# Performance work log

Measured on AMD Instinct MI355X. Metric: run time of the kernel, lower is better.

## Reference

```python
import jax, jax.numpy as jnp
import numpy as np

B, C_IN, C_OUT, DK, N = 4, 64, 64, 64, 4096

def setup_inputs() -> dict:
    key = jax.random.key(0)
    kx, kq, kk, kv = jax.random.split(key, 4)
    return {
        "x": jax.random.normal(kx, (B, C_IN, N), dtype=jnp.float32),
        "Wq": jax.random.normal(kq, (DK, C_IN), dtype=jnp.float32) * 0.1,
        "Wk": jax.random.normal(kk, (DK, C_IN), dtype=jnp.float32) * 0.1,
        "Wv": jax.random.normal(kv, (C_OUT, C_IN), dtype=jnp.float32) * 0.1,
    }

def reference(x, Wq, Wk, Wv):
    # Conv1d(kernel=1, bias=False) == channel matmul.
    q = jnp.einsum('dc,bcn->bnd', Wq, x)          # (B, N, dk)  (transpose(1,2))
    k = jnp.einsum('dc,bcn->bdn', Wk, x)          # (B, dk, N)
    v = jnp.einsum('oc,bcn->bon', Wv, x)          # (B, C_out, N)
    dk = q.shape[2]
    scores = jnp.einsum('bnd,bdm->bnm', q, k) / jnp.sqrt(jnp.asarray(dk, x.dtype))  # (B, N, N)
    attn = jax.nn.softmax(scores, axis=1)         # NOTE: softmax over dim=1 (columns), as in the torch code
    return jnp.einsum('bon,bnm->bom', v, attn)    # (B, C_out, N)
```

## Files before the change

### kernel.cpp

```cpp
#include <hip/hip_runtime.h>
#include <hip/hip_bf16.h>
#include <math.h>

#define N_ 4096
#define B_ 4
#define C_ 64
#define MT 64
#define NT 128
#define STEPS (N_ / NT)
#define QSCALE 0.1803368801111137f

typedef __attribute__((ext_vector_type(8))) short bf16x8;
typedef __attribute__((ext_vector_type(4))) float f32x4;
#define MFMA(a, b, c) __builtin_amdgcn_mfma_f32_16x16x32_bf16(a, b, c, 0, 0, 0)

#if __has_builtin(__builtin_amdgcn_exp2f)
#define EXP2(x) __builtin_amdgcn_exp2f(x)
#else
#define EXP2(x) __expf((x) * 0.6931471805599453f)
#endif

static __device__ __forceinline__ uint hi_bits(float f) {
    return (__float_as_uint(f) + 0x8000u) >> 16;
}
static __device__ __forceinline__ float hi_val(float f) {
    return __uint_as_float((__float_as_uint(f) + 0x8000u) & 0xFFFF0000u);
}

__global__ __launch_bounds__(256) void qkv_mfma(
    const float* __restrict__ x,  const float* __restrict__ Wq,
    const float* __restrict__ Wk, const float* __restrict__ Wv,
    ushort* __restrict__ Qh, ushort* __restrict__ Kh, ushort* __restrict__ Vh)
{
    __shared__ float xs[C_][33];

    const int b   = blockIdx.x / (N_ / 32);
    const int n0  = (blockIdx.x % (N_ / 32)) * 32;
    const int tid = threadIdx.x;
    const int w   = tid >> 6;
    const int l   = tid & 63;
    const int lr  = l & 15;
    const int lg  = l >> 4;

    #pragma unroll
    for (int it = 0; it < 2; ++it) {
        const int i = tid + it * 256;
        const int row = i >> 3, q = i & 7;
        const float4 a = *(const float4*)(x + ((size_t)b * C_ + row) * N_ + n0 + q * 4);
        xs[row][q * 4 + 0] = a.x; xs[row][q * 4 + 1] = a.y;
        xs[row][q * 4 + 2] = a.z; xs[row][q * 4 + 3] = a.w;
    }

    bf16x8 wh[3][2], wl[3][2];
    #pragma unroll
    for (int i = 0; i < 3; ++i) {
        const int rt  = w * 3 + i;
        const int mat = rt >> 2;
        const int dt  = rt & 3;
        const float* __restrict__ W = (mat == 0) ? Wq : ((mat == 1) ? Wk : Wv);
        const float scale = (mat == 0) ? QSCALE : 1.0f;
        #pragma unroll
        for (int ks = 0; ks < 2; ++ks) {
            const float4* p = (const float4*)(W + (dt * 16 + lr) * C_ + ks * 32 + lg * 8);
            float4 f0 = p[0], f1 = p[1];
            float v[8] = {f0.x, f0.y, f0.z, f0.w, f1.x, f1.y, f1.z, f1.w};
            bf16x8 ht, lt;
            #pragma unroll
            for (int j = 0; j < 8; ++j) {
                const float f = v[j] * scale;
                const float h = hi_val(f);
                ht[j] = (short)(__float_as_uint(h) >> 16);
                lt[j] = (short)hi_bits(f - h);
            }
            wh[i][ks] = ht; wl[i][ks] = lt;
        }
    }
    __syncthreads();

    #pragma unroll
    for (int nt = 0; nt < 2; ++nt) {
        bf16x8 xh[2], xl[2];
        #pragma unroll
        for (int ks = 0; ks < 2; ++ks) {
            bf16x8 ht, lt;
            #pragma unroll
            for (int j = 0; j < 8; ++j) {
                const float f = xs[ks * 32 + lg * 8 + j][nt * 16 + lr];
                const float h = hi_val(f);
                ht[j] = (short)(__float_as_uint(h) >> 16);
                lt[j] = (short)hi_bits(f - h);
            }
            xh[ks] = ht; xl[ks] = lt;
        }

        #pragma unroll
        for (int i = 0; i < 3; ++i) {
            const int rt  = w * 3 + i;
            const int mat = rt >> 2;
            const int dt  = rt & 3;
            f32x4 acc = (f32x4){0.f, 0.f, 0.f, 0.f};
            if (mat < 2) {
                #pragma unroll
                for (int ks = 0; ks < 2; ++ks) {
                    acc = MFMA(wh[i][ks], xh[ks], acc);
                    acc = MFMA(wh[i][ks], xl[ks], acc);
                    acc = MFMA(wl[i][ks], xh[ks], acc);
                }
                ushort* __restrict__ H = mat ? Kh : Qh;
                const size_t base = ((size_t)b * N_ + n0 + nt * 16 + lr) * C_ + dt * 16 + lg * 4;
                *(uint2*)(H + base) = make_uint2((hi_bits(acc[1]) << 16) | hi_bits(acc[0]),
                                                 (hi_bits(acc[3]) << 16) | hi_bits(acc[2]));
            } else {
                #pragma unroll
                for (int ks = 0; ks < 2; ++ks) {
                    acc = MFMA(xh[ks], wh[i][ks], acc);
                    acc = MFMA(xl[ks], wh[i][ks], acc);
                    acc = MFMA(xh[ks], wl[i][ks], acc);
                }
                const size_t base = ((size_t)b * C_ + dt * 16 + lr) * N_ + n0 + nt * 16 + lg * 4;
                *(uint2*)(Vh + base) = make_uint2((hi_bits(acc[1]) << 16) | hi_bits(acc[0]),
                                                  (hi_bits(acc[3]) << 16) | hi_bits(acc[2]));
            }
        }
    }
}

__global__ __launch_bounds__(256) void attn_mfma(
    const ushort* __restrict__ Qh, const ushort* __restrict__ Kh,
    const ushort* __restrict__ Vh, float* __restrict__ out)
{
    __shared__ ushort Em[2][MT * NT];
    __shared__ float red[4][MT];

    const int bid = blockIdx.x;
    const int b   = (bid & 7) >> 1;
    const int mt  = (bid & 1) + ((bid >> 3) << 1);
    const int tid = threadIdx.x;
    const int w   = tid >> 6;
    const int l   = tid & 63;
    const int lr  = l & 15;
    const int lg  = l >> 4;

    const int m0 = mt * MT;

    bf16x8 khf[4][2];
    #pragma unroll
    for (int f = 0; f < 4; ++f)
        #pragma unroll
        for (int ks = 0; ks < 2; ++ks)
            khf[f][ks] = *(const bf16x8*)(Kh + ((size_t)b * N_ + m0 + f * 16 + lr) * C_ + ks * 32 + lg * 8);

    f32x4 oacc[4];
    #pragma unroll
    for (int f = 0; f < 4; ++f) oacc[f] = (f32x4){0.f, 0.f, 0.f, 0.f};
    float den[4] = {0.f, 0.f, 0.f, 0.f};

    bf16x8 qcur[2][2];
    #pragma unroll
    for (int nt2 = 0; nt2 < 2; ++nt2)
        #pragma unroll
        for (int ks = 0; ks < 2; ++ks)
            qcur[nt2][ks] = *(const bf16x8*)(Qh + ((size_t)b * N_ + w * 32 + nt2 * 16 + lr) * C_ + ks * 32 + lg * 8);

    for (int t = 0; t < STEPS; ++t) {
        const int nbase = t * NT;
        const int buf   = t & 1;

        bf16x8 vh[4];
        #pragma unroll
        for (int ks = 0; ks < 4; ++ks)
            vh[ks] = *(const bf16x8*)(Vh + ((size_t)b * C_ + w * 16 + lr) * N_ + nbase + ks * 32 + lg * 8);

        f32x4 s2[2][4];
        #pragma unroll
        for (int nt2 = 0; nt2 < 2; ++nt2)
            #pragma unroll
            for (int f = 0; f < 4; ++f) s2[nt2][f] = (f32x4){0.f, 0.f, 0.f, 0.f};
        #pragma unroll
        for (int ks = 0; ks < 2; ++ks)
            #pragma unroll
            for (int nt2 = 0; nt2 < 2; ++nt2)
                #pragma unroll
                for (int f = 0; f < 4; ++f)
                    s2[nt2][f] = MFMA(qcur[nt2][ks], khf[f][ks], s2[nt2][f]);

        const int tn = (t + 1 < STEPS) ? (t + 1) : t;
        bf16x8 qnext[2][2];
        #pragma unroll
        for (int nt2 = 0; nt2 < 2; ++nt2)
            #pragma unroll
            for (int ks = 0; ks < 2; ++ks)
                qnext[nt2][ks] = *(const bf16x8*)(Qh + ((size_t)b * N_ + tn * NT + w * 32 + nt2 * 16 + lr) * C_ + ks * 32 + lg * 8);

        #pragma unroll
        for (int nt2 = 0; nt2 < 2; ++nt2)
            #pragma unroll
            for (int f = 0; f < 4; ++f) {
                const float e0 = EXP2(s2[nt2][f][0]);
                const float e1 = EXP2(s2[nt2][f][1]);
                const float e2 = EXP2(s2[nt2][f][2]);
                const float e3 = EXP2(s2[nt2][f][3]);
                den[f] += (e0 + e1) + (e2 + e3);
                const uint u0 = __float_as_uint(e0) + 0x8000u;
                const uint u1 = __float_as_uint(e1) + 0x8000u;
                const uint u2 = __float_as_uint(e2) + 0x8000u;
                const uint u3 = __float_as_uint(e3) + 0x8000u;
                const uint2 pk = make_uint2((u1 & 0xFFFF0000u) | (u0 >> 16),
                                            (u3 & 0xFFFF0000u) | (u2 >> 16));
                const int row = f * 16 + lr;
                const int g   = w * 4 + nt2 * 2 + (lg >> 1);
                *(uint2*)&Em[buf][row * NT + (((g + row) & 15) << 3) + ((lg & 1) << 2)] = pk;
            }
        __syncthreads();

        #pragma unroll
        for (int ks = 0; ks < 4; ++ks)
            #pragma unroll
            for (int f = 0; f < 4; ++f) {
                const int row = f * 16 + lr;
                const bf16x8 eb = *(const bf16x8*)&Em[buf][row * NT + (((ks * 4 + lg + row) & 15) << 3)];
                oacc[f] = MFMA(vh[ks], eb, oacc[f]);
            }

        #pragma unroll
        for (int nt2 = 0; nt2 < 2; ++nt2) {
            qcur[nt2][0] = qnext[nt2][0];
            qcur[nt2][1] = qnext[nt2][1];
        }
    }

    #pragma unroll
    for (int f = 0; f < 4; ++f) {
        den[f] += __shfl_xor(den[f], 16);
        den[f] += __shfl_xor(den[f], 32);
    }
    __syncthreads();
    if (lg == 0)
        #pragma unroll
        for (int f = 0; f < 4; ++f) red[w][f * 16 + lr] = den[f];
    __syncthreads();

    float inv[4];
    #pragma unroll
    for (int f = 0; f < 4; ++f) {
        const int m = f * 16 + lr;
        inv[f] = __builtin_amdgcn_rcpf(red[0][m] + red[1][m] + red[2][m] + red[3][m]);
    }

    #pragma unroll
    for (int f = 0; f < 4; ++f)
        #pragma unroll
        for (int r = 0; r < 4; ++r) {
            const int o = w * 16 + lg * 4 + r;
            out[((size_t)b * C_ + o) * N_ + m0 + f * 16 + lr] = oacc[f][r] * inv[f];
        }
}

extern "C" void kernel_launch(void* const* d_in, const int* in_sizes, int n_in,
                              void* d_out, int out_size, void* d_ws, size_t ws_size,
                              hipStream_t stream)
{
    const float* x  = (const float*)d_in[0];
    const float* Wq = (const float*)d_in[1];
    const float* Wk = (const float*)d_in[2];
    const float* Wv = (const float*)d_in[3];
    float* out = (float*)d_out;

    const size_t NE = (size_t)B_ * N_ * C_;
    ushort* Qh = (ushort*)d_ws;
    ushort* Kh = Qh + NE;
    ushort* Vh = Kh + NE;

    qkv_mfma<<<B_ * (N_ / 32), 256, 0, stream>>>(x, Wq, Wk, Wv, Qh, Kh, Vh);
    attn_mfma<<<B_ * (N_ / MT), 256, 0, stream>>>(Qh, Kh, Vh, out);
}
```

Baseline: 107.4 us.

## Warp-specialize attention kernel into score producer and PV consumer waves

Expands the attention block to 16 waves: 8 waves compute QK^T scores, exp and denominators for the next tile into a double-buffered LDS buffer, while 8 waves consume the current tile for the V·P MFMAs, splitting the n range in halves. Partial outputs from the two halves are reduced through LDS at the end. This aims to overlap exp/score work with the PV matmul and raise per-CU wave occupancy, at the cost of a larger block, extra LDS reduction and tighter register limits.

```diff
diff --git a/kernel.cpp b/kernel.cpp
--- a/kernel.cpp
+++ b/kernel.cpp
@@ -125,12 +125,12 @@
     }
 }
 
-__global__ __launch_bounds__(256) void attn_mfma(
+__global__ __launch_bounds__(1024) void attn_mfma(
     const ushort* __restrict__ Qh, const ushort* __restrict__ Kh,
     const ushort* __restrict__ Vh, float* __restrict__ out)
 {
     __shared__ ushort Em[2][MT * NT];
-    __shared__ float red[4][MT];
+    __shared__ float red[8][MT];
 
     const int bid = blockIdx.x;
     const int b   = (bid & 7) >> 1;
@@ -140,120 +140,152 @@
     const int l   = tid & 63;
     const int lr  = l & 15;
     const int lg  = l >> 4;
-
-    const int m0 = mt * MT;
+    const int m0  = mt * MT;
+
+    const bool sW = (w < 8);
+    const int pw  = w & 7;
+    const int ot  = pw & 3;
+    const int nh  = pw >> 2;
 
     bf16x8 khf[4][2];
-    #pragma unroll
-    for (int f = 0; f < 4; ++f)
-        #pragma unroll
-        for (int ks = 0; ks < 2; ++ks)
-            khf[f][ks] = *(const bf16x8*)(Kh + ((size_t)b * N_ + m0 + f * 16 + lr) * C_ + ks * 32 + lg * 8);
-
-    f32x4 oacc[4];
+    float  den[4] = {0.f, 0.f, 0.f, 0.f};
+    f32x4  oacc[4];
     #pragma unroll
     for (int f = 0; f < 4; ++f) oacc[f] = (f32x4){0.f, 0.f, 0.f, 0.f};
-    float den[4] = {0.f, 0.f, 0.f, 0.f};
-
-    bf16x8 qcur[2][2];
-    #pragma unroll
-    for (int nt2 = 0; nt2 < 2; ++nt2)
+    bf16x8 vcur[2];
+
+    if (sW) {
+        #pragma unroll
+        for (int f = 0; f < 4; ++f)
+            #pragma unroll
+            for (int ks = 0; ks < 2; ++ks)
+                khf[f][ks] = *(const bf16x8*)(Kh + ((size_t)b * N_ + m0 + f * 16 + lr) * C_ + ks * 32 + lg * 8);
+
+        bf16x8 q[2];
         #pragma unroll
         for (int ks = 0; ks < 2; ++ks)
-            qcur[nt2][ks] = *(const bf16x8*)(Qh + ((size_t)b * N_ + w * 32 + nt2 * 16 + lr) * C_ + ks * 32 + lg * 8);
+            q[ks] = *(const bf16x8*)(Qh + ((size_t)b * N_ + w * 16 + lr) * C_ + ks * 32 + lg * 8);
+        f32x4 s[4];
+        #pragma unroll
+        for (int f = 0; f < 4; ++f) s[f] = (f32x4){0.f, 0.f, 0.f, 0.f};
+        __builtin_amdgcn_s_setprio(1);
+        #pragma unroll
+        for (int ks = 0; ks < 2; ++ks)
+            #pragma unroll
+            for (int f = 0; f < 4; ++f) s[f] = MFMA(q[ks], khf[f][ks], s[f]);
+        __builtin_amdgcn_s_setprio(0);
+        #pragma unroll
+        for (int f = 0; f < 4; ++f) {
+            const float e0 = EXP2(s[f][0]), e1 = EXP2(s[f][1]);
+            const float e2 = EXP2(s[f][2]), e3 = EXP2(s[f][3]);
+            den[f] += (e0 + e1) + (e2 + e3);
+            const uint u0 = __float_as_uint(e0) + 0x8000u;
+            const uint u1 = __float_as_uint(e1) + 0x8000u;
+            const uint u2 = __float_as_uint(e2) + 0x8000u;
+            const uint u3 = __float_as_uint(e3) + 0x8000u;
+            const int row = f * 16 + lr;
+            const int g   = w * 2 + (lg >> 1);
+            *(uint2*)&Em[0][row * NT + (((g + row) & 15) << 3) + ((lg & 1) << 2)] =
+                make_uint2((u1 & 0xFFFF0000u) | (u0 >> 16), (u3 & 0xFFFF0000u) | (u2 >> 16));
+        }
+    } else {
+        #pragma unroll
+        for (int k2 = 0; k2 < 2; ++k2)
+            vcur[k2] = *(const bf16x8*)(Vh + ((size_t)b * C_ + ot * 16 + lr) * N_ + nh * 64 + k2 * 32 + lg * 8);
+    }
+    __syncthreads();
 
     for (int t = 0; t < STEPS; ++t) {
-        const int nbase = t * NT;
-        const int buf   = t & 1;
-
-        bf16x8 vh[4];
-        #pragma unroll
-        for (int ks = 0; ks < 4; ++ks)
-            vh[ks] = *(const bf16x8*)(Vh + ((size_t)b * C_ + w * 16 + lr) * N_ + nbase + ks * 32 + lg * 8);
-
-        f32x4 s2[2][4];
-        #pragma unroll
-        for (int nt2 = 0; nt2 < 2; ++nt2)
-            #pragma unroll
-            for (int f = 0; f < 4; ++f) s2[nt2][f] = (f32x4){0.f, 0.f, 0.f, 0.f};
-        #pragma unroll
-        for (int ks = 0; ks < 2; ++ks)
-            #pragma unroll
-            for (int nt2 = 0; nt2 < 2; ++nt2)
-                #pragma unroll
-                for (int f = 0; f < 4; ++f)
-                    s2[nt2][f] = MFMA(qcur[nt2][ks], khf[f][ks], s2[nt2][f]);
-
-        const int tn = (t + 1 < STEPS) ? (t + 1) : t;
-        bf16x8 qnext[2][2];
-        #pragma unroll
-        for (int nt2 = 0; nt2 < 2; ++nt2)
-            #pragma unroll
-            for (int ks = 0; ks < 2; ++ks)
-                qnext[nt2][ks] = *(const bf16x8*)(Qh + ((size_t)b * N_ + tn * NT + w * 32 + nt2 * 16 + lr) * C_ + ks * 32 + lg * 8);
-
-        #pragma unroll
-        for (int nt2 = 0; nt2 < 2; ++nt2)
-            #pragma unroll
-            for (int f = 0; f < 4; ++f) {
-                const float e0 = EXP2(s2[nt2][f][0]);
-                const float e1 = EXP2(s2[nt2][f][1]);
-                const float e2 = EXP2(s2[nt2][f][2]);
-                const float e3 = EXP2(s2[nt2][f][3]);
-                den[f] += (e0 + e1) + (e2 + e3);
-                const uint u0 = __float_as_uint(e0) + 0x8000u;
-                const uint u1 = __float_as_uint(e1) + 0x8000u;
-                const uint u2 = __float_as_uint(e2) + 0x8000u;
-                const uint u3 = __float_as_uint(e3) + 0x8000u;
-                const uint2 pk = make_uint2((u1 & 0xFFFF0000u) | (u0 >> 16),
-                                            (u3 & 0xFFFF0000u) | (u2 >> 16));
-                const int row = f * 16 + lr;
-                const int g   = w * 4 + nt2 * 2 + (lg >> 1);
-                *(uint2*)&Em[buf][row * NT + (((g + row) & 15) << 3) + ((lg & 1) << 2)] = pk;
-            }
+        if (sW) {
+            if (t + 1 < STEPS) {
+                bf16x8 q[2];
+                #pragma unroll
+                for (int ks = 0; ks < 2; ++ks)
+                    q[ks] = *(const bf16x8*)(Qh + ((size_t)b * N_ + (t + 1) * NT + w * 16 + lr) * C_ + ks * 32 + lg * 8);
+                f32x4 s[4];
+                #pragma unroll
+                for (int f = 0; f < 4; ++f) s[f] = (f32x4){0.f, 0.f, 0.f, 0.f};
+                __builtin_amdgcn_s_setprio(1);
+                #pragma unroll
+                for (int ks = 0; ks < 2; ++ks)
+                    #pragma unroll
+                    for (int f = 0; f < 4; ++f) s[f] = MFMA(q[ks], khf[f][ks], s[f]);
+                __builtin_amdgcn_s_setprio(0);
+                const int buf = (t + 1) & 1;
+                #pragma unroll
+                for (int f = 0; f < 4; ++f) {
+                    const float e0 = EXP2(s[f][0]), e1 = EXP2(s[f][1]);
+                    const float e2 = EXP2(s[f][2]), e3 = EXP2(s[f][3]);
+                    den[f] += (e0 + e1) + (e2 + e3);
+                    const uint u0 = __float_as_uint(e0) + 0x8000u;
+                    const uint u1 = __float_as_uint(e1) + 0x8000u;
+                    const uint u2 = __float_as_uint(e2) + 0x8000u;
+                    const uint u3 = __float_as_uint(e3) + 0x8000u;
+                    const int row = f * 16 + lr;
+                    const int g   = w * 2 + (lg >> 1);
+                    *(uint2*)&Em[buf][row * NT + (((g + row) & 15) << 3) + ((lg & 1) << 2)] =
+                        make_uint2((u1 & 0xFFFF0000u) | (u0 >> 16), (u3 & 0xFFFF0000u) | (u2 >> 16));
+                }
+            }
+        } else {
+            const int tv = (t + 1 < STEPS) ? t + 1 : t;
+            bf16x8 vnext[2];
+            #pragma unroll
+            for (int k2 = 0; k2 < 2; ++k2)
+                vnext[k2] = *(const bf16x8*)(Vh + ((size_t)b * C_ + ot * 16 + lr) * N_ + (size_t)tv * NT + nh * 64 + k2 * 32 + lg * 8);
+            __builtin_amdgcn_s_setprio(1);
+            #pragma unroll
+            for (int k2 = 0; k2 < 2; ++k2)
+                #pragma unroll
+                for (int f = 0; f < 4; ++f) {
+                    const int row = f * 16 + lr;
+                    const int lgc = (nh * 2 + k2) * 4 + lg;
+                    const bf16x8 eb = *(const bf16x8*)&Em[t & 1][row * NT + (((lgc + row) & 15) << 3)];
+                    oacc[f] = MFMA(vcur[k2], eb, oacc[f]);
+                }
+            __builtin_amdgcn_s_setprio(0);
+            vcur[0] = vnext[0]; vcur[1] = vnext[1];
+        }
         __syncthreads();
-
-        #pragma unroll
-        for (int ks = 0; ks < 4; ++ks)
-            #pragma unroll
-            for (int f = 0; f < 4; ++f) {
-                const int row = f * 16 + lr;
-                const bf16x8 eb = *(const bf16x8*)&Em[buf][row * NT + (((ks * 4 + lg + row) & 15) << 3)];
-                oacc[f] = MFMA(vh[ks], eb, oacc[f]);
-            }
-
-        #pragma unroll
-        for (int nt2 = 0; nt2 < 2; ++nt2) {
-            qcur[nt2][0] = qnext[nt2][0];
-            qcur[nt2][1] = qnext[nt2][1];
-        }
-    }
-
-    #pragma unroll
-    for (int f = 0; f < 4; ++f) {
-        den[f] += __shfl_xor(den[f], 16);
-        den[f] += __shfl_xor(den[f], 32);
+    }
+
+    if (sW) {
+        #pragma unroll
+        for (int f = 0; f < 4; ++f) {
+            den[f] += __shfl_xor(den[f], 16);
+            den[f] += __shfl_xor(den[f], 32);
+        }
+        if (lg == 0)
+            #pragma unroll
+            for (int f = 0; f < 4; ++f) red[w][f * 16 + lr] = den[f];
+    } else if (nh == 1) {
+        float* scr = (float*)&Em[0][0];
+        #pragma unroll
+        for (int f = 0; f < 4; ++f)
+            #pragma unroll
+            for (int r = 0; r < 4; ++r)
+                scr[(ot * 16 + lg * 4 + r) * 65 + f * 16 + lr] = oacc[f][r];
     }
     __syncthreads();
-    if (lg == 0)
-        #pragma unroll
-        for (int f = 0; f < 4; ++f) red[w][f * 16 + lr] = den[f];
-    __syncthreads();
-
-    float inv[4];
-    #pragma unroll
-    for (int f = 0; f < 4; ++f) {
-        const int m = f * 16 + lr;
-        inv[f] = __builtin_amdgcn_rcpf(red[0][m] + red[1][m] + red[2][m] + red[3][m]);
-    }
-
-    #pragma unroll
-    for (int f = 0; f < 4; ++f)
-        #pragma unroll
-        for (int r = 0; r < 4; ++r) {
-            const int o = w * 16 + lg * 4 + r;
-            out[((size_t)b * C_ + o) * N_ + m0 + f * 16 + lr] = oacc[f][r] * inv[f];
-        }
+
+    if (!sW && nh == 0) {
+        const float* scr = (const float*)&Em[0][0];
+        float inv[4];
+        #pragma unroll
+        for (int f = 0; f < 4; ++f) {
+            const int m = f * 16 + lr;
+            inv[f] = __builtin_amdgcn_rcpf(red[0][m] + red[1][m] + red[2][m] + red[3][m] +
+                                           red[4][m] + red[5][m] + red[6][m] + red[7][m]);
+        }
+        #pragma unroll
+        for (int f = 0; f < 4; ++f)
+            #pragma unroll
+            for (int r = 0; r < 4; ++r) {
+                const int o = ot * 16 + lg * 4 + r;
+                out[((size_t)b * C_ + o) * N_ + m0 + f * 16 + lr] =
+                    (oacc[f][r] + scr[o * 65 + f * 16 + lr]) * inv[f];
+            }
+    }
 }
 
 extern "C" void kernel_launch(void* const* d_in, const int* in_sizes, int n_in,
@@ -272,5 +304,5 @@
     ushort* Vh = Kh + NE;
 
     qkv_mfma<<<B_ * (N_ / 32), 256, 0, stream>>>(x, Wq, Wk, Wv, Qh, Kh, Vh);
-    attn_mfma<<<B_ * (N_ / MT), 256, 0, stream>>>(Qh, Kh, Vh, out);
-}
+    attn_mfma<<<B_ * (N_ / MT), 1024, 0, stream>>>(Qh, Kh, Vh, out);
+}
```

Result: slower. 110.0 us (+2.4%).

## Split attention key dimension across eight waves with 32x32 MFMA and register transpose

Applied to the files above, without the earlier changes.

The attention kernel now gives each block 32 output columns and splits the 4096-long reduction over 8 waves. Each wave computes scores with 32x32x16 bf16 MFMAs and transposes the exponentials into B-operand layout using cross-lane shuffles, so the LDS staging and per-step barrier are gone. A tree reduction through shared memory combines partial outputs and denominators at the end. This raises the grid to 512 blocks of 512 threads for more parallelism, but adds a reduction epilogue, higher register pressure and more redundant Q/V loads per block.

```diff
diff --git a/kernel.cpp b/kernel.cpp
--- a/kernel.cpp
+++ b/kernel.cpp
@@ -5,14 +5,18 @@
 #define N_ 4096
 #define B_ 4
 #define C_ 64
-#define MT 64
-#define NT 128
-#define STEPS (N_ / NT)
+#define WN 8
+#define NSEG (N_ / WN)
+#define ST2 (NSEG / 32)
 #define QSCALE 0.1803368801111137f
 
-typedef __attribute__((ext_vector_type(8))) short bf16x8;
-typedef __attribute__((ext_vector_type(4))) float f32x4;
-#define MFMA(a, b, c) __builtin_amdgcn_mfma_f32_16x16x32_bf16(a, b, c, 0, 0, 0)
+typedef __attribute__((ext_vector_type(8)))  short bf16x8;
+typedef __attribute__((ext_vector_type(4)))  float f32x4;
+typedef __attribute__((ext_vector_type(16))) float f32x16;
+typedef __attribute__((ext_vector_type(4)))  uint  u32x4;
+
+#define MFMA(a, b, c)   __builtin_amdgcn_mfma_f32_16x16x32_bf16(a, b, c, 0, 0, 0)
+#define MFMA32(a, b, c) __builtin_amdgcn_mfma_f32_32x32x16_bf16(a, b, c, 0, 0, 0)
 
 #if __has_builtin(__builtin_amdgcn_exp2f)
 #define EXP2(x) __builtin_amdgcn_exp2f(x)
@@ -25,6 +29,10 @@
 }
 static __device__ __forceinline__ float hi_val(float f) {
     return __uint_as_float((__float_as_uint(f) + 0x8000u) & 0xFFFF0000u);
+}
+static __device__ __forceinline__ uint pk2(float a, float b) {
+    return ((__float_as_uint(b) + 0x8000u) & 0xFFFF0000u) |
+           ((__float_as_uint(a) + 0x8000u) >> 16);
 }
 
 __global__ __launch_bounds__(256) void qkv_mfma(
@@ -125,12 +133,12 @@
     }
 }
 
-__global__ __launch_bounds__(256) void attn_mfma(
+__global__ __launch_bounds__(512, 4) void attn_mfma(
     const ushort* __restrict__ Qh, const ushort* __restrict__ Kh,
     const ushort* __restrict__ Vh, float* __restrict__ out)
 {
-    __shared__ ushort Em[2][MT * NT];
-    __shared__ float red[4][MT];
+    __shared__ float obuf[4][2048];
+    __shared__ float lred[WN][32];
 
     const int bid = blockIdx.x;
     const int b   = (bid & 7) >> 1;
@@ -138,122 +146,142 @@
     const int tid = threadIdx.x;
     const int w   = tid >> 6;
     const int l   = tid & 63;
-    const int lr  = l & 15;
-    const int lg  = l >> 4;
-
-    const int m0 = mt * MT;
-
-    bf16x8 khf[4][2];
-    #pragma unroll
-    for (int f = 0; f < 4; ++f)
-        #pragma unroll
-        for (int ks = 0; ks < 2; ++ks)
-            khf[f][ks] = *(const bf16x8*)(Kh + ((size_t)b * N_ + m0 + f * 16 + lr) * C_ + ks * 32 + lg * 8);
-
-    f32x4 oacc[4];
-    #pragma unroll
-    for (int f = 0; f < 4; ++f) oacc[f] = (f32x4){0.f, 0.f, 0.f, 0.f};
-    float den[4] = {0.f, 0.f, 0.f, 0.f};
-
-    bf16x8 qcur[2][2];
-    #pragma unroll
-    for (int nt2 = 0; nt2 < 2; ++nt2)
-        #pragma unroll
-        for (int ks = 0; ks < 2; ++ks)
-            qcur[nt2][ks] = *(const bf16x8*)(Qh + ((size_t)b * N_ + w * 32 + nt2 * 16 + lr) * C_ + ks * 32 + lg * 8);
-
-    for (int t = 0; t < STEPS; ++t) {
-        const int nbase = t * NT;
-        const int buf   = t & 1;
-
-        bf16x8 vh[4];
-        #pragma unroll
-        for (int ks = 0; ks < 4; ++ks)
-            vh[ks] = *(const bf16x8*)(Vh + ((size_t)b * C_ + w * 16 + lr) * N_ + nbase + ks * 32 + lg * 8);
-
-        f32x4 s2[2][4];
-        #pragma unroll
-        for (int nt2 = 0; nt2 < 2; ++nt2)
-            #pragma unroll
-            for (int f = 0; f < 4; ++f) s2[nt2][f] = (f32x4){0.f, 0.f, 0.f, 0.f};
-        #pragma unroll
-        for (int ks = 0; ks < 2; ++ks)
-            #pragma unroll
-            for (int nt2 = 0; nt2 < 2; ++nt2)
-                #pragma unroll
-                for (int f = 0; f < 4; ++f)
-                    s2[nt2][f] = MFMA(qcur[nt2][ks], khf[f][ks], s2[nt2][f]);
-
-        const int tn = (t + 1 < STEPS) ? (t + 1) : t;
-        bf16x8 qnext[2][2];
-        #pragma unroll
-        for (int nt2 = 0; nt2 < 2; ++nt2)
+    const int lm  = l & 31;
+    const int hi  = l >> 5;
+    const int m0  = mt * 32;
+
+    bf16x8 kb[4];
+    #pragma unroll
+    for (int dt = 0; dt < 4; ++dt)
+        kb[dt] = *(const bf16x8*)(Kh + ((size_t)b * N_ + m0 + lm) * C_ + dt * 16 + hi * 8);
+
+    f32x16 occ0, occ1;
+    #pragma unroll
+    for (int r = 0; r < 16; ++r) { occ0[r] = 0.f; occ1[r] = 0.f; }
+    float den = 0.f;
+
+    const int n0 = w * NSEG;
+    const ushort* __restrict__ Qb = Qh + (size_t)b * N_ * C_;
+    const ushort* __restrict__ Vb = Vh + (size_t)b * C_ * N_;
+
+    for (int t = 0; t < ST2; ++t) {
+        const int nb = n0 + t * 32;
+
+        bf16x8 va[4];
+        #pragma unroll
+        for (int ot = 0; ot < 2; ++ot)
             #pragma unroll
             for (int ks = 0; ks < 2; ++ks)
-                qnext[nt2][ks] = *(const bf16x8*)(Qh + ((size_t)b * N_ + tn * NT + w * 32 + nt2 * 16 + lr) * C_ + ks * 32 + lg * 8);
-
-        #pragma unroll
-        for (int nt2 = 0; nt2 < 2; ++nt2)
-            #pragma unroll
-            for (int f = 0; f < 4; ++f) {
-                const float e0 = EXP2(s2[nt2][f][0]);
-                const float e1 = EXP2(s2[nt2][f][1]);
-                const float e2 = EXP2(s2[nt2][f][2]);
-                const float e3 = EXP2(s2[nt2][f][3]);
-                den[f] += (e0 + e1) + (e2 + e3);
-                const uint u0 = __float_as_uint(e0) + 0x8000u;
-                const uint u1 = __float_as_uint(e1) + 0x8000u;
-                const uint u2 = __float_as_uint(e2) + 0x8000u;
-                const uint u3 = __float_as_uint(e3) + 0x8000u;
-                const uint2 pk = make_uint2((u1 & 0xFFFF0000u) | (u0 >> 16),
-                                            (u3 & 0xFFFF0000u) | (u2 >> 16));
-                const int row = f * 16 + lr;
-                const int g   = w * 4 + nt2 * 2 + (lg >> 1);
-                *(uint2*)&Em[buf][row * NT + (((g + row) & 15) << 3) + ((lg & 1) << 2)] = pk;
-            }
-        __syncthreads();
-
-        #pragma unroll
-        for (int ks = 0; ks < 4; ++ks)
-            #pragma unroll
-            for (int f = 0; f < 4; ++f) {
-                const int row = f * 16 + lr;
-                const bf16x8 eb = *(const bf16x8*)&Em[buf][row * NT + (((ks * 4 + lg + row) & 15) << 3)];
-                oacc[f] = MFMA(vh[ks], eb, oacc[f]);
-            }
-
-        #pragma unroll
-        for (int nt2 = 0; nt2 < 2; ++nt2) {
-            qcur[nt2][0] = qnext[nt2][0];
-            qcur[nt2][1] = qnext[nt2][1];
-        }
-    }
-
-    #pragma unroll
-    for (int f = 0; f < 4; ++f) {
-        den[f] += __shfl_xor(den[f], 16);
-        den[f] += __shfl_xor(den[f], 32);
-    }
-    __syncthreads();
-    if (lg == 0)
-        #pragma unroll
-        for (int f = 0; f < 4; ++f) red[w][f * 16 + lr] = den[f];
-    __syncthreads();
-
-    float inv[4];
-    #pragma unroll
-    for (int f = 0; f < 4; ++f) {
-        const int m = f * 16 + lr;
-        inv[f] = __builtin_amdgcn_rcpf(red[0][m] + red[1][m] + red[2][m] + red[3][m]);
-    }
-
-    #pragma unroll
-    for (int f = 0; f < 4; ++f)
-        #pragma unroll
-        for (int r = 0; r < 4; ++r) {
-            const int o = w * 16 + lg * 4 + r;
-            out[((size_t)b * C_ + o) * N_ + m0 + f * 16 + lr] = oacc[f][r] * inv[f];
-        }
+                va[ot * 2 + ks] = *(const bf16x8*)(Vb + ((size_t)(ot * 32 + lm)) * N_ + nb + ks * 16 + hi * 8);
+
+        bf16x8 qa[4];
+        #pragma unroll
+        for (int dt = 0; dt < 4; ++dt)
+            qa[dt] = *(const bf16x8*)(Qb + ((size_t)(nb + lm)) * C_ + dt * 16 + hi * 8);
+
+        f32x16 s;
+        #pragma unroll
+        for (int r = 0; r < 16; ++r) s[r] = 0.f;
+        #pragma unroll
+        for (int dt = 0; dt < 4; ++dt)
+            s = MFMA32(qa[dt], kb[dt], s);
+
+        float e[16];
+        #pragma unroll
+        for (int r = 0; r < 16; ++r) e[r] = EXP2(s[r]);
+        #pragma unroll
+        for (int r = 0; r < 16; r += 4)
+            den += ((e[r] + e[r + 1]) + (e[r + 2] + e[r + 3]));
+        uint P[8];
+        #pragma unroll
+        for (int g = 0; g < 8; ++g) P[g] = pk2(e[2 * g], e[2 * g + 1]);
+
+        uint sw[8];
+        #pragma unroll
+        for (int g = 0; g < 8; ++g) sw[g] = __shfl_xor(P[g], 32);
+
+        u32x4 t0, t1;
+        t0.x = hi ? sw[2] : P[0];  t0.y = hi ? sw[3] : P[1];
+        t0.z = hi ? P[2]  : sw[0]; t0.w = hi ? P[3]  : sw[1];
+        t1.x = hi ? sw[6] : P[4];  t1.y = hi ? sw[7] : P[5];
+        t1.z = hi ? P[6]  : sw[4]; t1.w = hi ? P[7]  : sw[5];
+        const bf16x8 eb0 = __builtin_bit_cast(bf16x8, t0);
+        const bf16x8 eb1 = __builtin_bit_cast(bf16x8, t1);
+
+        occ0 = MFMA32(va[0], eb0, occ0);
+        occ0 = MFMA32(va[1], eb1, occ0);
+        occ1 = MFMA32(va[2], eb0, occ1);
+        occ1 = MFMA32(va[3], eb1, occ1);
+    }
+
+    den += __shfl_xor(den, 32);
+    if (l < 32) lred[w][lm] = den;
+
+    if (w >= 4) {
+        float* dst = obuf[w - 4];
+        #pragma unroll
+        for (int r = 0; r < 16; ++r) {
+            const int o = (r & 3) + 8 * (r >> 2) + 4 * hi;
+            dst[o * 32 + lm]        = occ0[r];
+            dst[(o + 32) * 32 + lm] = occ1[r];
+        }
+    }
+    __syncthreads();
+    if (w < 4) {
+        const float* src = obuf[w];
+        #pragma unroll
+        for (int r = 0; r < 16; ++r) {
+            const int o = (r & 3) + 8 * (r >> 2) + 4 * hi;
+            occ0[r] += src[o * 32 + lm];
+            occ1[r] += src[(o + 32) * 32 + lm];
+        }
+    }
+    __syncthreads();
+    if (w == 2 || w == 3) {
+        float* dst = obuf[w - 2];
+        #pragma unroll
+        for (int r = 0; r < 16; ++r) {
+            const int o = (r & 3) + 8 * (r >> 2) + 4 * hi;
+            dst[o * 32 + lm]        = occ0[r];
+            dst[(o + 32) * 32 + lm] = occ1[r];
+        }
+    }
+    __syncthreads();
+    if (w < 2) {
+        const float* src = obuf[w];
+        #pragma unroll
+        for (int r = 0; r < 16; ++r) {
+            const int o = (r & 3) + 8 * (r >> 2) + 4 * hi;
+            occ0[r] += src[o * 32 + lm];
+            occ1[r] += src[(o + 32) * 32 + lm];
+        }
+    }
+    __syncthreads();
+    if (w == 1) {
+        float* dst = obuf[0];
+        #pragma unroll
+        for (int r = 0; r < 16; ++r) {
+            const int o = (r & 3) + 8 * (r >> 2) + 4 * hi;
+            dst[o * 32 + lm]        = occ0[r];
+            dst[(o + 32) * 32 + lm] = occ1[r];
+        }
+    }
+    __syncthreads();
+    if (w == 0) {
+        float dtot = 0.f;
+        #pragma unroll
+        for (int i = 0; i < WN; ++i) dtot += lred[i][lm];
+        const float inv = __builtin_amdgcn_rcpf(dtot);
+        const float* src = obuf[0];
+        #pragma unroll
+        for (int r = 0; r < 16; ++r) {
+            const int o = (r & 3) + 8 * (r >> 2) + 4 * hi;
+            out[((size_t)b * C_ + o) * N_ + m0 + lm] =
+                (occ0[r] + src[o * 32 + lm]) * inv;
+            out[((size_t)b * C_ + o + 32) * N_ + m0 + lm] =
+                (occ1[r] + src[(o + 32) * 32 + lm]) * inv;
+        }
+    }
 }
 
 extern "C" void kernel_launch(void* const* d_in, const int* in_sizes, int n_in,
@@ -272,5 +300,5 @@
     ushort* Vh = Kh + NE;
 
     qkv_mfma<<<B_ * (N_ / 32), 256, 0, stream>>>(x, Wq, Wk, Wv, Qh, Kh, Vh);
-    attn_mfma<<<B_ * (N_ / MT), 256, 0, stream>>>(Qh, Kh, Vh, out);
-}
+    attn_mfma<<<B_ * (N_ / 32), 512, 0, stream>>>(Qh, Kh, Vh, out);
+}
```

New measurement: 130.4 us. 21.4% more time.

## Split attention reduction over N across two wave groups with smaller M tiles

Applied to the files above, without the earlier changes.

Halves the output-column tile to 32 and doubles the block to 512 threads. Two groups of four waves each take half of the N reduction range, and their partial outputs and denominators are combined through shared memory at the end. MFMA sections are wrapped in s_setprio to favour matrix issue. The grid grows to 512 blocks to fill more CUs, at the cost of re-reading Q and V per smaller tile and an extra cross-group reduction.

```diff
diff --git a/kernel.cpp b/kernel.cpp
--- a/kernel.cpp
+++ b/kernel.cpp
@@ -5,9 +5,10 @@
 #define N_ 4096
 #define B_ 4
 #define C_ 64
-#define MT 64
+#define MT 32
 #define NT 128
-#define STEPS (N_ / NT)
+#define HSEG 2048
+#define STEPS (HSEG / NT)
 #define QSCALE 0.1803368801111137f
 
 typedef __attribute__((ext_vector_type(8))) short bf16x8;
@@ -125,64 +126,68 @@
     }
 }
 
-__global__ __launch_bounds__(256) void attn_mfma(
+__global__ __launch_bounds__(512, 4) void attn_mfma(
     const ushort* __restrict__ Qh, const ushort* __restrict__ Kh,
     const ushort* __restrict__ Vh, float* __restrict__ out)
 {
-    __shared__ ushort Em[2][MT * NT];
-    __shared__ float red[4][MT];
+    __shared__ ushort Em[2][2][MT * NT];
+    __shared__ float red[8][MT];
 
     const int bid = blockIdx.x;
     const int b   = (bid & 7) >> 1;
     const int mt  = (bid & 1) + ((bid >> 3) << 1);
     const int tid = threadIdx.x;
     const int w   = tid >> 6;
+    const int g2  = w >> 2;
+    const int w4  = w & 3;
     const int l   = tid & 63;
     const int lr  = l & 15;
     const int lg  = l >> 4;
-
-    const int m0 = mt * MT;
-
-    bf16x8 khf[4][2];
-    #pragma unroll
-    for (int f = 0; f < 4; ++f)
+    const int m0  = mt * MT;
+    const int nG  = g2 * HSEG;
+
+    bf16x8 khf[2][2];
+    #pragma unroll
+    for (int f = 0; f < 2; ++f)
         #pragma unroll
         for (int ks = 0; ks < 2; ++ks)
             khf[f][ks] = *(const bf16x8*)(Kh + ((size_t)b * N_ + m0 + f * 16 + lr) * C_ + ks * 32 + lg * 8);
 
-    f32x4 oacc[4];
-    #pragma unroll
-    for (int f = 0; f < 4; ++f) oacc[f] = (f32x4){0.f, 0.f, 0.f, 0.f};
-    float den[4] = {0.f, 0.f, 0.f, 0.f};
+    f32x4 oacc[2];
+    oacc[0] = (f32x4){0.f, 0.f, 0.f, 0.f};
+    oacc[1] = (f32x4){0.f, 0.f, 0.f, 0.f};
+    float den[2] = {0.f, 0.f};
 
     bf16x8 qcur[2][2];
     #pragma unroll
     for (int nt2 = 0; nt2 < 2; ++nt2)
         #pragma unroll
         for (int ks = 0; ks < 2; ++ks)
-            qcur[nt2][ks] = *(const bf16x8*)(Qh + ((size_t)b * N_ + w * 32 + nt2 * 16 + lr) * C_ + ks * 32 + lg * 8);
+            qcur[nt2][ks] = *(const bf16x8*)(Qh + ((size_t)b * N_ + nG + w4 * 32 + nt2 * 16 + lr) * C_ + ks * 32 + lg * 8);
 
     for (int t = 0; t < STEPS; ++t) {
-        const int nbase = t * NT;
+        const int nbase = nG + t * NT;
         const int buf   = t & 1;
 
         bf16x8 vh[4];
         #pragma unroll
         for (int ks = 0; ks < 4; ++ks)
-            vh[ks] = *(const bf16x8*)(Vh + ((size_t)b * C_ + w * 16 + lr) * N_ + nbase + ks * 32 + lg * 8);
-
-        f32x4 s2[2][4];
+            vh[ks] = *(const bf16x8*)(Vh + ((size_t)b * C_ + w4 * 16 + lr) * N_ + nbase + ks * 32 + lg * 8);
+
+        f32x4 s2[2][2];
         #pragma unroll
         for (int nt2 = 0; nt2 < 2; ++nt2)
             #pragma unroll
-            for (int f = 0; f < 4; ++f) s2[nt2][f] = (f32x4){0.f, 0.f, 0.f, 0.f};
+            for (int f = 0; f < 2; ++f) s2[nt2][f] = (f32x4){0.f, 0.f, 0.f, 0.f};
+        __builtin_amdgcn_s_setprio(1);
         #pragma unroll
         for (int ks = 0; ks < 2; ++ks)
             #pragma unroll
             for (int nt2 = 0; nt2 < 2; ++nt2)
                 #pragma unroll
-                for (int f = 0; f < 4; ++f)
+                for (int f = 0; f < 2; ++f)
                     s2[nt2][f] = MFMA(qcur[nt2][ks], khf[f][ks], s2[nt2][f]);
+        __builtin_amdgcn_s_setprio(0);
 
         const int tn = (t + 1 < STEPS) ? (t + 1) : t;
         bf16x8 qnext[2][2];
@@ -190,12 +195,12 @@
         for (int nt2 = 0; nt2 < 2; ++nt2)
             #pragma unroll
             for (int ks = 0; ks < 2; ++ks)
-                qnext[nt2][ks] = *(const bf16x8*)(Qh + ((size_t)b * N_ + tn * NT + w * 32 + nt2 * 16 + lr) * C_ + ks * 32 + lg * 8);
+                qnext[nt2][ks] = *(const bf16x8*)(Qh + ((size_t)b * N_ + nG + tn * NT + w4 * 32 + nt2 * 16 + lr) * C_ + ks * 32 + lg * 8);
 
         #pragma unroll
         for (int nt2 = 0; nt2 < 2; ++nt2)
             #pragma unroll
-            for (int f = 0; f < 4; ++f) {
+            for (int f = 0; f < 2; ++f) {
                 const float e0 = EXP2(s2[nt2][f][0]);
                 const float e1 = EXP2(s2[nt2][f][1]);
                 const float e2 = EXP2(s2[nt2][f][2]);
@@ -205,22 +210,23 @@
                 const uint u1 = __float_as_uint(e1) + 0x8000u;
                 const uint u2 = __float_as_uint(e2) + 0x8000u;
                 const uint u3 = __float_as_uint(e3) + 0x8000u;
-                const uint2 pk = make_uint2((u1 & 0xFFFF0000u) | (u0 >> 16),
-                                            (u3 & 0xFFFF0000u) | (u2 >> 16));
                 const int row = f * 16 + lr;
-                const int g   = w * 4 + nt2 * 2 + (lg >> 1);
-                *(uint2*)&Em[buf][row * NT + (((g + row) & 15) << 3) + ((lg & 1) << 2)] = pk;
+                const int g   = w4 * 4 + nt2 * 2 + (lg >> 1);
+                *(uint2*)&Em[g2][buf][row * NT + (((g + row) & 15) << 3) + ((lg & 1) << 2)] =
+                    make_uint2((u1 & 0xFFFF0000u) | (u0 >> 16), (u3 & 0xFFFF0000u) | (u2 >> 16));
             }
         __syncthreads();
 
+        __builtin_amdgcn_s_setprio(1);
         #pragma unroll
         for (int ks = 0; ks < 4; ++ks)
             #pragma unroll
-            for (int f = 0; f < 4; ++f) {
+            for (int f = 0; f < 2; ++f) {
                 const int row = f * 16 + lr;
-                const bf16x8 eb = *(const bf16x8*)&Em[buf][row * NT + (((ks * 4 + lg + row) & 15) << 3)];
+                const bf16x8 eb = *(const bf16x8*)&Em[g2][buf][row * NT + (((ks * 4 + lg + row) & 15) << 3)];
                 oacc[f] = MFMA(vh[ks], eb, oacc[f]);
             }
+        __builtin_amdgcn_s_setprio(0);
 
         #pragma unroll
         for (int nt2 = 0; nt2 < 2; ++nt2) {
@@ -229,31 +235,44 @@
         }
     }
 
-    #pragma unroll
-    for (int f = 0; f < 4; ++f) {
+    __syncthreads();
+
+    #pragma unroll
+    for (int f = 0; f < 2; ++f) {
         den[f] += __shfl_xor(den[f], 16);
         den[f] += __shfl_xor(den[f], 32);
     }
+    if (lg == 0) {
+        red[w][lr]      = den[0];
+        red[w][16 + lr] = den[1];
+    }
+    float* scr = (float*)&Em[1][0][0];
+    if (w >= 4) {
+        #pragma unroll
+        for (int f = 0; f < 2; ++f)
+            #pragma unroll
+            for (int r = 0; r < 4; ++r)
+                scr[(w4 * 16 + lg * 4 + r) * 33 + f * 16 + lr] = oacc[f][r];
+    }
     __syncthreads();
-    if (lg == 0)
-        #pragma unroll
-        for (int f = 0; f < 4; ++f) red[w][f * 16 + lr] = den[f];
-    __syncthreads();
-
-    float inv[4];
-    #pragma unroll
-    for (int f = 0; f < 4; ++f) {
-        const int m = f * 16 + lr;
-        inv[f] = __builtin_amdgcn_rcpf(red[0][m] + red[1][m] + red[2][m] + red[3][m]);
-    }
-
-    #pragma unroll
-    for (int f = 0; f < 4; ++f)
-        #pragma unroll
-        for (int r = 0; r < 4; ++r) {
-            const int o = w * 16 + lg * 4 + r;
-            out[((size_t)b * C_ + o) * N_ + m0 + f * 16 + lr] = oacc[f][r] * inv[f];
-        }
+
+    if (w < 4) {
+        float inv[2];
+        #pragma unroll
+        for (int f = 0; f < 2; ++f) {
+            const int m = f * 16 + lr;
+            inv[f] = __builtin_amdgcn_rcpf(red[0][m] + red[1][m] + red[2][m] + red[3][m] +
+                                           red[4][m] + red[5][m] + red[6][m] + red[7][m]);
+        }
+        #pragma unroll
+        for (int f = 0; f < 2; ++f)
+            #pragma unroll
+            for (int r = 0; r < 4; ++r) {
+                const int o = w4 * 16 + lg * 4 + r;
+                out[((size_t)b * C_ + o) * N_ + m0 + f * 16 + lr] =
+                    (oacc[f][r] + scr[o * 33 + f * 16 + lr]) * inv[f];
+            }
+    }
 }
 
 extern "C" void kernel_launch(void* const* d_in, const int* in_sizes, int n_in,
@@ -272,5 +291,5 @@
     ushort* Vh = Kh + NE;
 
     qkv_mfma<<<B_ * (N_ / 32), 256, 0, stream>>>(x, Wq, Wk, Wv, Qh, Kh, Vh);
-    attn_mfma<<<B_ * (N_ / MT), 256, 0, stream>>>(Qh, Kh, Vh, out);
-}
+    attn_mfma<<<B_ * (N_ / MT), 512, 0, stream>>>(Qh, Kh, Vh, out);
+}
```

Result: slower. 127.2 us (+18.4%).
